# Optimization experiments

Measured on AMD Instinct MI355X. Metric: run time of the kernel, lower is better.

The kernel has to match this reference:

```python
import jax, jax.numpy as jnp
import numpy as np

N = 100_000      # nodes
E = 1_600_000    # edges (before self-loops)
IN_C = 500
HID = 128
OUT_C = 64
L = 8
ALPHA = 0.1
THETA = 0.5


def setup_inputs() -> dict:
    key = jax.random.key(0)
    ks = jax.random.split(key, 6)
    x = jax.random.normal(ks[0], (N, IN_C), dtype=jnp.float32)
    edge_index = jax.random.randint(ks[1], (2, E), 0, N, dtype=jnp.int32)
    s0 = 1.0 / np.sqrt(IN_C)
    W_in = jax.random.uniform(ks[2], (IN_C, HID), jnp.float32, -s0, s0)
    b_in = jnp.zeros((HID,), jnp.float32)
    sh = 1.0 / np.sqrt(HID)
    W_conv = jax.random.uniform(ks[3], (L, HID, HID), jnp.float32, -sh, sh)
    W_out = jax.random.uniform(ks[4], (HID, OUT_C), jnp.float32, -sh, sh)
    b_out = jnp.zeros((OUT_C,), jnp.float32)
    return {"x": x, "edge_index": edge_index, "W_in": W_in, "b_in": b_in,
            "W_conv": W_conv, "W_out": W_out, "b_out": b_out}


def reference(x, edge_index, W_in, b_in, W_conv, W_out, b_out):
    # dropout is identity in eval mode
    loop = jnp.arange(N, dtype=edge_index.dtype)
    src = jnp.concatenate([edge_index[0], loop])  # add self-loops (gcn_norm)
    dst = jnp.concatenate([edge_index[1], loop])
    deg = jax.ops.segment_sum(jnp.ones_like(src, dtype=x.dtype), dst, num_segments=N)
    dinv = jnp.where(deg > 0, jax.lax.rsqrt(deg), 0.0)
    norm = dinv[src] * dinv[dst]  # symmetric normalization coeffs per edge

    h = jax.nn.relu(x @ W_in + b_in)
    h0 = h  # initial residual
    for l in range(L):
        beta = float(np.log(THETA / (l + 1) + 1.0))
        agg = jax.ops.segment_sum(h[src] * norm[:, None], dst, num_segments=N)  # Ahat @ h
        z = (1.0 - ALPHA) * agg + ALPHA * h0
        h = jax.nn.relu((1.0 - beta) * z + beta * (z @ W_conv[l]))
    return h @ W_out + b_out
```

## Files before the change

### kernel.cpp

```cpp
#include <hip/hip_runtime.h>
#include <hip/hip_fp16.h>
#include <cmath>

#define NN 100000
#define EE 1600000
#define INC 500
#define HIDC 128
#define OUTC 64
#define NLAYER 8
#define NW32 3125
#define NB16 6250
#define FUSE_BLKS 7032

typedef float f32x4 __attribute__((ext_vector_type(4)));
typedef __bf16 bf16x8 __attribute__((ext_vector_type(8)));
typedef _Float16 f16x8 __attribute__((ext_vector_type(8)));
typedef short s16x4 __attribute__((ext_vector_type(4)));
typedef short s16x8 __attribute__((ext_vector_type(8)));

__device__ __forceinline__ unsigned short f2bf_rn(float f) {
  unsigned u = __float_as_uint(f);
  unsigned r = u + 0x7fffu + ((u >> 16) & 1u);
  return (unsigned short)(r >> 16);
}
__device__ __forceinline__ float bf2f(unsigned short h) {
  return __uint_as_float(((unsigned)h) << 16);
}

__device__ __forceinline__ int fraddr(int row, int k, int Kp) {
  return (row >> 4) * (Kp * 16) + (k >> 3) * 128 + (row & 15) * 8 + (k & 7);
}


__global__ void k_count_deg(const int* __restrict__ dst, int* __restrict__ deg, int E) {
  int e = blockIdx.x * blockDim.x + threadIdx.x;
  if (e < E) atomicAdd(&deg[dst[e]], 1);
}

__global__ void k_scan_block_sums(const int* __restrict__ deg, int* __restrict__ bsum, int n) {
  __shared__ int sm[256];
  int i = blockIdx.x * 256 + threadIdx.x;
  int v = (i < n) ? deg[i] + 1 : 0;
  sm[threadIdx.x] = v;
  __syncthreads();
  for (int s = 128; s > 0; s >>= 1) {
    if (threadIdx.x < s) sm[threadIdx.x] += sm[threadIdx.x + s];
    __syncthreads();
  }
  if (threadIdx.x == 0) bsum[blockIdx.x] = sm[0];
}

__global__ void k_scan_partials(int* __restrict__ bsum, int nb) {
  __shared__ int sm[512];
  int t = threadIdx.x;
  sm[t] = (t < nb) ? bsum[t] : 0;
  __syncthreads();
  for (int s = 1; s < 512; s <<= 1) {
    int v = (t >= s) ? sm[t - s] : 0;
    __syncthreads();
    sm[t] += v;
    __syncthreads();
  }
  if (t < nb) bsum[t] = (t == 0) ? 0 : sm[t - 1];
}

__global__ void k_scan_final(const int* __restrict__ deg, const int* __restrict__ bsum,
                             int* __restrict__ row_ptr, int n) {
  __shared__ int sm[256];
  int i = blockIdx.x * 256 + threadIdx.x;
  int v = (i < n) ? deg[i] + 1 : 0;
  sm[threadIdx.x] = v;
  __syncthreads();
  for (int s = 1; s < 256; s <<= 1) {
    int u = (threadIdx.x >= s) ? sm[threadIdx.x - s] : 0;
    __syncthreads();
    sm[threadIdx.x] += u;
    __syncthreads();
  }
  if (i < n) row_ptr[i] = bsum[blockIdx.x] + sm[threadIdx.x] - v;
}

__global__ void k_init_rows(const int* __restrict__ deg, const int* __restrict__ row_ptr,
                            int* __restrict__ cursor, int* __restrict__ col,
                            float* __restrict__ dinv, int n) {
  int i = blockIdx.x * blockDim.x + threadIdx.x;
  if (i < n) {
    int rp = row_ptr[i];
    col[rp] = i;
    cursor[i] = rp + 1;
    dinv[i] = rsqrtf((float)(deg[i] + 1));
  }
}


__global__ void k_prep_wfin(const float* __restrict__ W, unsigned short* __restrict__ fh,
                            unsigned short* __restrict__ fl) {
  int i = blockIdx.x * 256 + threadIdx.x;
  if (i >= HIDC * 512) return;
  int n = i / 512, k = i % 512;
  float v = (k < INC) ? W[(size_t)k * HIDC + n] : 0.f;
  unsigned short h = f2bf_rn(v);
  unsigned short l = f2bf_rn(v - bf2f(h));
  int a = fraddr(n, k, 512);
  fh[a] = h;
  fl[a] = l;
}


__global__ void k_prep_wf16(const float* __restrict__ W, __half* __restrict__ f,
                            int K, int N, float idc, float ws) {
  int i = blockIdx.x * 256 + threadIdx.x;
  if (i >= N * K) return;
  int n = i / K, k = i % K;
  float v = ws * W[(size_t)k * N + n] + ((k == n) ? idc : 0.f);
  f[fraddr(n, k, K)] = __float2half(v);
}


__global__ void __launch_bounds__(256) k_fill_gemm(
    const int* __restrict__ src, const int* __restrict__ dst,
    int* __restrict__ cursor, int* __restrict__ col,
    const float* __restrict__ A, const unsigned short* __restrict__ Bfh,
    const unsigned short* __restrict__ Bfl, const float* __restrict__ bias,
    __half* __restrict__ C16u, __half* __restrict__ C16s,
    const float* __restrict__ dinv) {
  __shared__ __align__(16) unsigned short Ah[128 * 40];
  __shared__ __align__(16) unsigned short Al[128 * 40];
  int bid = blockIdx.x;
  int tid = threadIdx.x;

  if (bid % 9 != 0) {
    int fidx = bid - (bid / 9 + 1);
    int e = fidx * 256 + tid;
    if (e < EE) {
      int pos = atomicAdd(&cursor[dst[e]], 1);
      col[pos] = src[e];
    }
    return;
  }

  int blk = bid / 9;
  int wid = tid >> 6, lane = tid & 63;
  int wr = wid >> 1, wc = wid & 1;
  int lr = lane & 15, kg = lane >> 4;
  int row0 = blk * 128;

  f32x4 acc[4][4];
#pragma unroll
  for (int m = 0; m < 4; ++m)
#pragma unroll
    for (int n = 0; n < 4; ++n) acc[m][n] = {0.f, 0.f, 0.f, 0.f};

  float4 va[4];
  auto issue_loads = [&](int kt) {
#pragma unroll
    for (int p = 0; p < 4; ++p) {
      int idx = tid + p * 256;
      int r = idx >> 3, kq = idx & 7;
      int gr = row0 + r, gk = kt + kq * 4;
      va[p] = make_float4(0.f, 0.f, 0.f, 0.f);
      if (gr < NN && gk < INC) va[p] = *reinterpret_cast<const float4*>(&A[(size_t)gr * INC + gk]);
    }
  };

  issue_loads(0);
  for (int kt = 0; kt < 512; kt += 32) {
#pragma unroll
    for (int p = 0; p < 4; ++p) {
      int idx = tid + p * 256;
      int r = idx >> 3, kq = idx & 7;
      const float* vp = &va[p].x;
      s16x4 h4, l4;
#pragma unroll
      for (int e = 0; e < 4; ++e) {
        unsigned short h = f2bf_rn(vp[e]);
        h4[e] = (short)h;
        l4[e] = (short)f2bf_rn(vp[e] - bf2f(h));
      }
      *reinterpret_cast<s16x4*>(&Ah[r * 40 + kq * 4]) = h4;
      *reinterpret_cast<s16x4*>(&Al[r * 40 + kq * 4]) = l4;
    }
    __syncthreads();
    if (kt + 32 < 512) issue_loads(kt + 32);

    bf16x8 afh[4], afl[4];
#pragma unroll
    for (int m = 0; m < 4; ++m) {
      int r = wr * 64 + m * 16 + lr;
      afh[m] = *reinterpret_cast<const bf16x8*>(&Ah[r * 40 + kg * 8]);
      afl[m] = *reinterpret_cast<const bf16x8*>(&Al[r * 40 + kg * 8]);
    }
#pragma unroll
    for (int n = 0; n < 4; ++n) {
      size_t bb = (size_t)(wc * 4 + n) * 8192 + (size_t)(kt / 8 + kg) * 128 + lr * 8;
      bf16x8 bh = *reinterpret_cast<const bf16x8*>(&Bfh[bb]);
      bf16x8 bl = *reinterpret_cast<const bf16x8*>(&Bfl[bb]);
#pragma unroll
      for (int m = 0; m < 4; ++m) {
        acc[m][n] = __builtin_amdgcn_mfma_f32_16x16x32_bf16(afh[m], bh, acc[m][n], 0, 0, 0);
        acc[m][n] = __builtin_amdgcn_mfma_f32_16x16x32_bf16(afl[m], bh, acc[m][n], 0, 0, 0);
        acc[m][n] = __builtin_amdgcn_mfma_f32_16x16x32_bf16(afh[m], bl, acc[m][n], 0, 0, 0);
      }
    }
    __syncthreads();
  }

#pragma unroll
  for (int m = 0; m < 4; ++m) {
#pragma unroll
    for (int n = 0; n < 4; ++n) {
      int gc = wc * 64 + n * 16 + lr;
#pragma unroll
      for (int q = 0; q < 4; ++q) {
        int gr = row0 + wr * 64 + m * 16 + kg * 4 + q;
        if (gr < NN) {
          float v = fmaxf(acc[m][n][q] + bias[gc], 0.f);
          C16u[(size_t)gr * HIDC + gc] = __float2half(v);
          C16s[(size_t)gr * HIDC + gc] = __float2half(v * dinv[gr]);
        }
      }
    }
  }
}


template <int EPI>
__global__ void __launch_bounds__(1024) k_layer(
    const __half* __restrict__ hs, const __half* __restrict__ h0u,
    const __half* __restrict__ Bf,
    const int* __restrict__ row_ptr, const int* __restrict__ deg,
    const int* __restrict__ col, const float* __restrict__ dinv,
    __half* __restrict__ Cs, __half* __restrict__ Cff) {
  __shared__ __half zb[16 * 128];
  int wv = threadIdx.x >> 6, lane = threadIdx.x & 63;
  int g = lane >> 4;
  int fl = lane & 15;
  int row0 = blockIdx.x * 16;
  int node = row0 + wv;

  int start = row_ptr[node];
  int cnt = deg[node] + 1;
  int nch = (cnt + 3) >> 2;

  float acc[8];
#pragma unroll
  for (int j = 0; j < 8; ++j) acc[j] = 0.f;

  auto load_chunk = [&](int ch, s16x8& v, float& m) {
    int e = ch * 4 + g;
    bool valid = e < cnt;
    int c = col[start + (valid ? e : 0)];
    m = valid ? 1.f : 0.f;
    v = *reinterpret_cast<const s16x8*>(&hs[(size_t)c * HIDC + fl * 8]);
  };

  s16x8 curv; float curm;
  load_chunk(0, curv, curm);
  for (int ch = 0; ch < nch; ++ch) {
    s16x8 nv = {}; float nm = 0.f;
    if (ch + 1 < nch) load_chunk(ch + 1, nv, nm);
    const __half2* hp = reinterpret_cast<const __half2*>(&curv);
#pragma unroll
    for (int j = 0; j < 4; ++j) {
      float2 f = __half22float2(hp[j]);
      acc[2 * j]     = fmaf(curm, f.x, acc[2 * j]);
      acc[2 * j + 1] = fmaf(curm, f.y, acc[2 * j + 1]);
    }
    curv = nv; curm = nm;
  }

#pragma unroll
  for (int j = 0; j < 8; ++j) {
    acc[j] += __shfl_xor(acc[j], 16, 64);
    acc[j] += __shfl_xor(acc[j], 32, 64);
  }

  if (g == 0) {
    float dr = dinv[node] * 0.9f;
    s16x8 r0 = *reinterpret_cast<const s16x8*>(&h0u[(size_t)node * HIDC + fl * 8]);
    const __half2* r0p = reinterpret_cast<const __half2*>(&r0);
    f16x8 w;
#pragma unroll
    for (int j = 0; j < 4; ++j) {
      float2 f0 = __half22float2(r0p[j]);
      w[2 * j]     = (_Float16)fmaf(dr, acc[2 * j],     0.1f * f0.x);
      w[2 * j + 1] = (_Float16)fmaf(dr, acc[2 * j + 1], 0.1f * f0.y);
    }
    *reinterpret_cast<f16x8*>(&zb[wv * 128 + ((fl * 8) ^ ((wv & 7) << 3))]) = w;
  }
  __syncthreads();

  if (wv < 8) {
    int lr = lane & 15, kg = lane >> 4;
    f32x4 c = {0.f, 0.f, 0.f, 0.f};
    const __half* Bb = Bf + wv * 2048 + kg * 128 + lr * 8;
#pragma unroll
    for (int kt = 0; kt < 4; ++kt) {
      f16x8 a = *reinterpret_cast<const f16x8*>(
          &zb[lr * 128 + ((kt * 32 + kg * 8) ^ ((lr & 7) << 3))]);
      f16x8 b = *reinterpret_cast<const f16x8*>(Bb + kt * 512);
      c = __builtin_amdgcn_mfma_f32_16x16x32_f16(a, b, c, 0, 0, 0);
    }
    int gc = wv * 16 + lr;
#pragma unroll
    for (int q = 0; q < 4; ++q) {
      int gr = row0 + kg * 4 + q;
      float v = fmaxf(c[q], 0.f);
      if (EPI == 0) {
        Cs[(size_t)gr * HIDC + gc] = __float2half(v * dinv[gr]);
      } else {
        Cff[fraddr(gr, gc, HIDC)] = __float2half(v);
      }
    }
  }
}


__global__ void __launch_bounds__(256) k_fgemm_out(
    const __half* __restrict__ Af, const __half* __restrict__ Bf,
    const float* __restrict__ bias, float* __restrict__ Cf) {
  constexpr int NF = OUTC / 16;
  int wv = threadIdx.x >> 6, lane = threadIdx.x & 63;
  int lr = lane & 15, kg = lane >> 4;
  int w32 = blockIdx.x * 4 + wv;
  if (w32 >= NW32) return;
  int row0 = w32 * 32;

  f32x4 acc[2][NF];
#pragma unroll
  for (int m = 0; m < 2; ++m)
#pragma unroll
    for (int n = 0; n < NF; ++n) acc[m][n] = {0.f, 0.f, 0.f, 0.f};

  const __half* Ab = Af + (size_t)(w32 * 2) * 2048 + kg * 128 + lr * 8;
  const __half* Bb = Bf + kg * 128 + lr * 8;

#pragma unroll
  for (int kt = 0; kt < 4; ++kt) {
    f16x8 a0 = *reinterpret_cast<const f16x8*>(Ab + kt * 512);
    f16x8 a1 = *reinterpret_cast<const f16x8*>(Ab + 2048 + kt * 512);
#pragma unroll
    for (int n = 0; n < NF; ++n) {
      f16x8 b = *reinterpret_cast<const f16x8*>(Bb + n * 2048 + kt * 512);
      acc[0][n] = __builtin_amdgcn_mfma_f32_16x16x32_f16(a0, b, acc[0][n], 0, 0, 0);
      acc[1][n] = __builtin_amdgcn_mfma_f32_16x16x32_f16(a1, b, acc[1][n], 0, 0, 0);
    }
  }

#pragma unroll
  for (int m = 0; m < 2; ++m) {
#pragma unroll
    for (int q = 0; q < 4; ++q) {
      int gr = row0 + m * 16 + kg * 4 + q;
#pragma unroll
      for (int n = 0; n < NF; ++n) {
        int gc = n * 16 + lr;
        Cf[(size_t)gr * OUTC + gc] = acc[m][n][q] + bias[gc];
      }
    }
  }
}


extern "C" void kernel_launch(void* const* d_in, const int* in_sizes, int n_in,
                              void* d_out, int out_size, void* d_ws, size_t ws_size,
                              hipStream_t stream) {
  const float* x     = (const float*)d_in[0];
  const int*   ei    = (const int*)d_in[1];
  const float* W_in  = (const float*)d_in[2];
  const float* b_in  = (const float*)d_in[3];
  const float* W_cv  = (const float*)d_in[4];
  const float* W_out = (const float*)d_in[5];
  const float* b_out = (const float*)d_in[6];
  float* out = (float*)d_out;

  char* ws = (char*)d_ws;
  size_t off = 0;
  auto alloc = [&](size_t bytes) {
    char* p = ws + off;
    off = (off + bytes + 255) & ~(size_t)255;
    return p;
  };
  int*    deg     = (int*)alloc((size_t)NN * 4);
  int*    row_ptr = (int*)alloc((size_t)NN * 4);
  int*    cursor  = (int*)alloc((size_t)NN * 4);
  int*    bsum    = (int*)alloc(512 * 4);
  float*  dinv    = (float*)alloc((size_t)NN * 4);
  int*    col     = (int*)alloc((size_t)(EE + NN) * 4);
  __half* h016u   = (__half*)alloc((size_t)NN * HIDC * 2);
  __half* h016s   = (__half*)alloc((size_t)NN * HIDC * 2);
  __half* hsA     = (__half*)alloc((size_t)NN * HIDC * 2);
  __half* hsB     = (__half*)alloc((size_t)NN * HIDC * 2);
  __half* hf      = (__half*)alloc((size_t)NN * HIDC * 2);
  __half* wcv16   = (__half*)alloc((size_t)NLAYER * HIDC * HIDC * 2);
  __half* wout16  = (__half*)alloc((size_t)OUTC * HIDC * 2);
  unsigned short* win_h = (unsigned short*)alloc((size_t)HIDC * 512 * 2);
  unsigned short* win_l = (unsigned short*)alloc((size_t)HIDC * 512 * 2);

  const int* srcp = ei;
  const int* dstp = ei + EE;

  hipMemsetAsync(deg, 0, (size_t)NN * 4, stream);
  k_count_deg<<<(EE + 255) / 256, 256, 0, stream>>>(dstp, deg, EE);
  int nb = (NN + 255) / 256;
  k_scan_block_sums<<<nb, 256, 0, stream>>>(deg, bsum, NN);
  k_scan_partials<<<1, 512, 0, stream>>>(bsum, nb);
  k_scan_final<<<nb, 256, 0, stream>>>(deg, bsum, row_ptr, NN);
  k_init_rows<<<(NN + 255) / 256, 256, 0, stream>>>(deg, row_ptr, cursor, col, dinv, NN);

  k_prep_wfin<<<(HIDC * 512 + 255) / 256, 256, 0, stream>>>(W_in, win_h, win_l);
  for (int l = 0; l < NLAYER; ++l) {
    float beta = logf(0.5f / (float)(l + 1) + 1.0f);
    k_prep_wf16<<<(HIDC * HIDC + 255) / 256, 256, 0, stream>>>(
        W_cv + (size_t)l * HIDC * HIDC, wcv16 + (size_t)l * HIDC * HIDC,
        HIDC, HIDC, 1.0f - beta, beta);
  }
  k_prep_wf16<<<(OUTC * HIDC + 255) / 256, 256, 0, stream>>>(W_out, wout16, HIDC, OUTC,
                                                             0.f, 1.f);

  k_fill_gemm<<<FUSE_BLKS, 256, 0, stream>>>(srcp, dstp, cursor, col,
                                             x, win_h, win_l, b_in,
                                             h016u, h016s, dinv);

  const __half* hcur = h016s;
  for (int l = 0; l < NLAYER; ++l) {
    const __half* wl = wcv16 + (size_t)l * HIDC * HIDC;
    if (l < NLAYER - 1) {
      __half* tgt = (l & 1) ? hsB : hsA;
      k_layer<0><<<NB16, 1024, 0, stream>>>(hcur, h016u, wl, row_ptr, deg, col, dinv,
                                            tgt, nullptr);
      hcur = tgt;
    } else {
      k_layer<1><<<NB16, 1024, 0, stream>>>(hcur, h016u, wl, row_ptr, deg, col, dinv,
                                            nullptr, hf);
    }
  }
  k_fgemm_out<<<(NW32 + 3) / 4, 256, 0, stream>>>(hf, wout16, b_out, out);
}
```

Measured before the change: 1.022 ms.

## Fuse degree count with input GEMM, XCD-partition CSR fill, fuse output GEMM

```diff
diff --git a/kernel.cpp b/kernel.cpp
--- a/kernel.cpp
+++ b/kernel.cpp
@@ -8,9 +8,11 @@
 #define HIDC 128
 #define OUTC 64
 #define NLAYER 8
-#define NW32 3125
 #define NB16 6250
-#define FUSE_BLKS 7032
+#define NPX 12500
+#define GEMM_BLKS 782
+#define CNT_BLKS 50000
+#define CG_BLKS (GEMM_BLKS + CNT_BLKS)
 
 typedef float f32x4 __attribute__((ext_vector_type(4)));
 typedef __bf16 bf16x8 __attribute__((ext_vector_type(8)));
@@ -31,11 +33,6 @@
   return (row >> 4) * (Kp * 16) + (k >> 3) * 128 + (row & 15) * 8 + (k & 7);
 }
 
-
-__global__ void k_count_deg(const int* __restrict__ dst, int* __restrict__ deg, int E) {
-  int e = blockIdx.x * blockDim.x + threadIdx.x;
-  if (e < E) atomicAdd(&deg[dst[e]], 1);
-}
 
 __global__ void k_scan_block_sums(const int* __restrict__ deg, int* __restrict__ bsum, int n) {
   __shared__ int sm[256];
@@ -89,6 +86,38 @@
     col[rp] = i;
     cursor[i] = rp + 1;
     dinv[i] = rsqrtf((float)(deg[i] + 1));
+  }
+}
+
+__global__ void __launch_bounds__(256) k_scale(
+    const __half* __restrict__ hu, const float* __restrict__ dinv,
+    __half* __restrict__ hsc) {
+  int i = blockIdx.x * 256 + threadIdx.x;
+  int gr = i >> 4, part = i & 15;
+  if (gr >= NN) return;
+  float dv = dinv[gr];
+  s16x8 v = *reinterpret_cast<const s16x8*>(&hu[(size_t)gr * HIDC + part * 8]);
+  const __half2* vp = reinterpret_cast<const __half2*>(&v);
+  f16x8 w;
+#pragma unroll
+  for (int j = 0; j < 4; ++j) {
+    float2 f = __half22float2(vp[j]);
+    w[2 * j]     = (_Float16)(f.x * dv);
+    w[2 * j + 1] = (_Float16)(f.y * dv);
+  }
+  *reinterpret_cast<f16x8*>(&hsc[(size_t)gr * HIDC + part * 8]) = w;
+}
+
+__global__ void __launch_bounds__(256) k_fill_x(
+    const int* __restrict__ src, const int* __restrict__ dst,
+    int* __restrict__ cursor, int* __restrict__ col) {
+  int chunk = blockIdx.x >> 3;
+  int xcd = blockIdx.x & 7;
+  int e = chunk * 256 + threadIdx.x;
+  int d = dst[e];
+  if (d / NPX == xcd) {
+    int pos = atomicAdd(&cursor[d], 1);
+    col[pos] = src[e];
   }
 }
 
@@ -117,29 +146,27 @@
 }
 
 
-__global__ void __launch_bounds__(256) k_fill_gemm(
-    const int* __restrict__ src, const int* __restrict__ dst,
-    int* __restrict__ cursor, int* __restrict__ col,
+__global__ void __launch_bounds__(256) k_count_gemm(
+    const int* __restrict__ dst, int* __restrict__ deg,
     const float* __restrict__ A, const unsigned short* __restrict__ Bfh,
     const unsigned short* __restrict__ Bfl, const float* __restrict__ bias,
-    __half* __restrict__ C16u, __half* __restrict__ C16s,
-    const float* __restrict__ dinv) {
+    __half* __restrict__ C16u) {
   __shared__ __align__(16) unsigned short Ah[128 * 40];
   __shared__ __align__(16) unsigned short Al[128 * 40];
   int bid = blockIdx.x;
   int tid = threadIdx.x;
 
-  if (bid % 9 != 0) {
-    int fidx = bid - (bid / 9 + 1);
-    int e = fidx * 256 + tid;
-    if (e < EE) {
-      int pos = atomicAdd(&cursor[dst[e]], 1);
-      col[pos] = src[e];
-    }
+  if (bid >= GEMM_BLKS) {
+    int o = bid - GEMM_BLKS;
+    int chunk = o >> 3;
+    int xcd = bid & 7;
+    int e = chunk * 256 + tid;
+    int d = dst[e];
+    if (d / NPX == xcd) atomicAdd(&deg[d], 1);
     return;
   }
 
-  int blk = bid / 9;
+  int blk = bid;
   int wid = tid >> 6, lane = tid & 63;
   int wr = wid >> 1, wc = wid & 1;
   int lr = lane & 15, kg = lane >> 4;
@@ -216,7 +243,6 @@
         if (gr < NN) {
           float v = fmaxf(acc[m][n][q] + bias[gc], 0.f);
           C16u[(size_t)gr * HIDC + gc] = __float2half(v);
-          C16s[(size_t)gr * HIDC + gc] = __float2half(v * dinv[gr]);
         }
       }
     }
@@ -230,7 +256,9 @@
     const __half* __restrict__ Bf,
     const int* __restrict__ row_ptr, const int* __restrict__ deg,
     const int* __restrict__ col, const float* __restrict__ dinv,
-    __half* __restrict__ Cs, __half* __restrict__ Cff) {
+    __half* __restrict__ Cs,
+    const __half* __restrict__ Bf2, const float* __restrict__ bias2,
+    float* __restrict__ outp) {
   __shared__ __half zb[16 * 128];
   int wv = threadIdx.x >> 6, lane = threadIdx.x & 63;
   int g = lane >> 4;
@@ -240,33 +268,38 @@
 
   int start = row_ptr[node];
   int cnt = deg[node] + 1;
-  int nch = (cnt + 3) >> 2;
 
   float acc[8];
 #pragma unroll
   for (int j = 0; j < 8; ++j) acc[j] = 0.f;
 
-  auto load_chunk = [&](int ch, s16x8& v, float& m) {
-    int e = ch * 4 + g;
-    bool valid = e < cnt;
-    int c = col[start + (valid ? e : 0)];
-    m = valid ? 1.f : 0.f;
-    v = *reinterpret_cast<const s16x8*>(&hs[(size_t)c * HIDC + fl * 8]);
-  };
-
-  s16x8 curv; float curm;
-  load_chunk(0, curv, curm);
-  for (int ch = 0; ch < nch; ++ch) {
-    s16x8 nv = {}; float nm = 0.f;
-    if (ch + 1 < nch) load_chunk(ch + 1, nv, nm);
-    const __half2* hp = reinterpret_cast<const __half2*>(&curv);
-#pragma unroll
-    for (int j = 0; j < 4; ++j) {
-      float2 f = __half22float2(hp[j]);
-      acc[2 * j]     = fmaf(curm, f.x, acc[2 * j]);
-      acc[2 * j + 1] = fmaf(curm, f.y, acc[2 * j + 1]);
-    }
-    curv = nv; curm = nm;
+  for (int base = 0; base < cnt; base += 64) {
+    int rem = cnt - base;
+    if (rem > 64) rem = 64;
+    int myc = col[start + base + (lane < rem ? lane : 0)];
+    int nch = (rem + 3) >> 2;
+
+    auto get = [&](int ch, s16x8& v, float& m) {
+      int e = ch * 4 + g;
+      int c = __shfl(myc, e & 63, 64);
+      m = (e < rem) ? 1.f : 0.f;
+      v = *reinterpret_cast<const s16x8*>(&hs[(size_t)c * HIDC + fl * 8]);
+    };
+
+    s16x8 curv; float curm;
+    get(0, curv, curm);
+    for (int ch = 0; ch < nch; ++ch) {
+      s16x8 nv = {}; float nm = 0.f;
+      if (ch + 1 < nch) get(ch + 1, nv, nm);
+      const __half2* hp = reinterpret_cast<const __half2*>(&curv);
+#pragma unroll
+      for (int j = 0; j < 4; ++j) {
+        float2 f = __half22float2(hp[j]);
+        acc[2 * j]     = fmaf(curm, f.x, acc[2 * j]);
+        acc[2 * j + 1] = fmaf(curm, f.y, acc[2 * j + 1]);
+      }
+      curv = nv; curm = nm;
+    }
   }
 
 #pragma unroll
@@ -290,9 +323,9 @@
   }
   __syncthreads();
 
+  int lr = lane & 15, kg = lane >> 4;
+  f32x4 c = {0.f, 0.f, 0.f, 0.f};
   if (wv < 8) {
-    int lr = lane & 15, kg = lane >> 4;
-    f32x4 c = {0.f, 0.f, 0.f, 0.f};
     const __half* Bb = Bf + wv * 2048 + kg * 128 + lr * 8;
 #pragma unroll
     for (int kt = 0; kt < 4; ++kt) {
@@ -301,61 +334,44 @@
       f16x8 b = *reinterpret_cast<const f16x8*>(Bb + kt * 512);
       c = __builtin_amdgcn_mfma_f32_16x16x32_f16(a, b, c, 0, 0, 0);
     }
-    int gc = wv * 16 + lr;
-#pragma unroll
-    for (int q = 0; q < 4; ++q) {
-      int gr = row0 + kg * 4 + q;
-      float v = fmaxf(c[q], 0.f);
-      if (EPI == 0) {
+  }
+
+  if (EPI == 0) {
+    if (wv < 8) {
+      int gc = wv * 16 + lr;
+#pragma unroll
+      for (int q = 0; q < 4; ++q) {
+        int gr = row0 + kg * 4 + q;
+        float v = fmaxf(c[q], 0.f);
         Cs[(size_t)gr * HIDC + gc] = __float2half(v * dinv[gr]);
-      } else {
-        Cff[fraddr(gr, gc, HIDC)] = __float2half(v);
-      }
-    }
-  }
-}
-
-
-__global__ void __launch_bounds__(256) k_fgemm_out(
-    const __half* __restrict__ Af, const __half* __restrict__ Bf,
-    const float* __restrict__ bias, float* __restrict__ Cf) {
-  constexpr int NF = OUTC / 16;
-  int wv = threadIdx.x >> 6, lane = threadIdx.x & 63;
-  int lr = lane & 15, kg = lane >> 4;
-  int w32 = blockIdx.x * 4 + wv;
-  if (w32 >= NW32) return;
-  int row0 = w32 * 32;
-
-  f32x4 acc[2][NF];
-#pragma unroll
-  for (int m = 0; m < 2; ++m)
-#pragma unroll
-    for (int n = 0; n < NF; ++n) acc[m][n] = {0.f, 0.f, 0.f, 0.f};
-
-  const __half* Ab = Af + (size_t)(w32 * 2) * 2048 + kg * 128 + lr * 8;
-  const __half* Bb = Bf + kg * 128 + lr * 8;
-
-#pragma unroll
-  for (int kt = 0; kt < 4; ++kt) {
-    f16x8 a0 = *reinterpret_cast<const f16x8*>(Ab + kt * 512);
-    f16x8 a1 = *reinterpret_cast<const f16x8*>(Ab + 2048 + kt * 512);
-#pragma unroll
-    for (int n = 0; n < NF; ++n) {
-      f16x8 b = *reinterpret_cast<const f16x8*>(Bb + n * 2048 + kt * 512);
-      acc[0][n] = __builtin_amdgcn_mfma_f32_16x16x32_f16(a0, b, acc[0][n], 0, 0, 0);
-      acc[1][n] = __builtin_amdgcn_mfma_f32_16x16x32_f16(a1, b, acc[1][n], 0, 0, 0);
-    }
-  }
-
-#pragma unroll
-  for (int m = 0; m < 2; ++m) {
-#pragma unroll
-    for (int q = 0; q < 4; ++q) {
-      int gr = row0 + m * 16 + kg * 4 + q;
-#pragma unroll
-      for (int n = 0; n < NF; ++n) {
-        int gc = n * 16 + lr;
-        Cf[(size_t)gr * OUTC + gc] = acc[m][n][q] + bias[gc];
+      }
+    }
+  } else {
+    __syncthreads();
+    if (wv < 8) {
+      int gc = wv * 16 + lr;
+#pragma unroll
+      for (int q = 0; q < 4; ++q) {
+        int r = kg * 4 + q;
+        zb[(gc >> 3) * 128 + r * 8 + (gc & 7)] = __float2half(fmaxf(c[q], 0.f));
+      }
+    }
+    __syncthreads();
+    if (wv < 4) {
+      f32x4 o = {0.f, 0.f, 0.f, 0.f};
+      const __half* Bb2 = Bf2 + wv * 2048 + kg * 128 + lr * 8;
+#pragma unroll
+      for (int kt = 0; kt < 4; ++kt) {
+        f16x8 a = *reinterpret_cast<const f16x8*>(&zb[(kt * 4 + kg) * 128 + lr * 8]);
+        f16x8 b = *reinterpret_cast<const f16x8*>(Bb2 + kt * 512);
+        o = __builtin_amdgcn_mfma_f32_16x16x32_f16(a, b, o, 0, 0, 0);
+      }
+      int gc = wv * 16 + lr;
+      float bv = bias2[gc];
+#pragma unroll
+      for (int q = 0; q < 4; ++q) {
+        int gr = row0 + kg * 4 + q;
+        outp[(size_t)gr * OUTC + gc] = o[q] + bv;
       }
     }
   }
@@ -391,7 +407,6 @@
   __half* h016s   = (__half*)alloc((size_t)NN * HIDC * 2);
   __half* hsA     = (__half*)alloc((size_t)NN * HIDC * 2);
   __half* hsB     = (__half*)alloc((size_t)NN * HIDC * 2);
-  __half* hf      = (__half*)alloc((size_t)NN * HIDC * 2);
   __half* wcv16   = (__half*)alloc((size_t)NLAYER * HIDC * HIDC * 2);
   __half* wout16  = (__half*)alloc((size_t)OUTC * HIDC * 2);
   unsigned short* win_h = (unsigned short*)alloc((size_t)HIDC * 512 * 2);
@@ -401,12 +416,6 @@
   const int* dstp = ei + EE;
 
   hipMemsetAsync(deg, 0, (size_t)NN * 4, stream);
-  k_count_deg<<<(EE + 255) / 256, 256, 0, stream>>>(dstp, deg, EE);
-  int nb = (NN + 255) / 256;
-  k_scan_block_sums<<<nb, 256, 0, stream>>>(deg, bsum, NN);
-  k_scan_partials<<<1, 512, 0, stream>>>(bsum, nb);
-  k_scan_final<<<nb, 256, 0, stream>>>(deg, bsum, row_ptr, NN);
-  k_init_rows<<<(NN + 255) / 256, 256, 0, stream>>>(deg, row_ptr, cursor, col, dinv, NN);
 
   k_prep_wfin<<<(HIDC * 512 + 255) / 256, 256, 0, stream>>>(W_in, win_h, win_l);
   for (int l = 0; l < NLAYER; ++l) {
@@ -418,9 +427,17 @@
   k_prep_wf16<<<(OUTC * HIDC + 255) / 256, 256, 0, stream>>>(W_out, wout16, HIDC, OUTC,
                                                              0.f, 1.f);
 
-  k_fill_gemm<<<FUSE_BLKS, 256, 0, stream>>>(srcp, dstp, cursor, col,
-                                             x, win_h, win_l, b_in,
-                                             h016u, h016s, dinv);
+  k_count_gemm<<<CG_BLKS, 256, 0, stream>>>(dstp, deg, x, win_h, win_l, b_in, h016u);
+
+  int nb = (NN + 255) / 256;
+  k_scan_block_sums<<<nb, 256, 0, stream>>>(deg, bsum, NN);
+  k_scan_partials<<<1, 512, 0, stream>>>(bsum, nb);
+  k_scan_final<<<nb, 256, 0, stream>>>(deg, bsum, row_ptr, NN);
+  k_init_rows<<<(NN + 255) / 256, 256, 0, stream>>>(deg, row_ptr, cursor, col, dinv, NN);
+
+  k_scale<<<(NN * 16 + 255) / 256, 256, 0, stream>>>(h016u, dinv, h016s);
+
+  k_fill_x<<<CNT_BLKS, 256, 0, stream>>>(srcp, dstp, cursor, col);
 
   const __half* hcur = h016s;
   for (int l = 0; l < NLAYER; ++l) {
@@ -428,12 +445,11 @@
     if (l < NLAYER - 1) {
       __half* tgt = (l & 1) ? hsB : hsA;
       k_layer<0><<<NB16, 1024, 0, stream>>>(hcur, h016u, wl, row_ptr, deg, col, dinv,
-                                            tgt, nullptr);
+                                            tgt, nullptr, nullptr, nullptr);
       hcur = tgt;
     } else {
       k_layer<1><<<NB16, 1024, 0, stream>>>(hcur, h016u, wl, row_ptr, deg, col, dinv,
-                                            nullptr, hf);
-    }
-  }
-  k_fgemm_out<<<(NW32 + 3) / 4, 256, 0, stream>>>(hf, wout16, b_out, out);
-}
+                                            nullptr, wout16, b_out, out);
+    }
+  }
+}
```

After: 915.5 us. -10.4%, faster.
